# Kernel optimization log

Measured on AMD Instinct MI355X. Metric: run time of the kernel, lower is better.

The kernel has to match this reference:

```python
import jax, jax.numpy as jnp
import numpy as np

TRUNK = 128  # hard-coded trunk_size in the Triton kernels


def setup_inputs() -> dict:
    key = jax.random.key(0)
    kq, kk, kv = jax.random.split(key, 3)
    N, D = 262144, 64
    Q = jax.random.normal(kq, (N, D), dtype=jnp.float32)
    K = jax.random.normal(kk, (N, D), dtype=jnp.float32)
    V = jax.random.normal(kv, (N, D), dtype=jnp.float32)
    return {"Q": Q, "K": K, "V": V}


def reference(Q, K, V):
    # Faithful to the Triton module:
    # 1) intra kernel overwrites Q in-place with, per trunk t:
    #      Q_t <- Q_t @ (V_t^T K_t)^T = Q_t @ K_t^T @ V_t
    # 2) inter kernel accumulates global state S = sum_t V_t^T K_t = V^T K (fp32)
    # 3) final output = Q_intra @ S
    N, D = Q.shape
    dtype = Q.dtype
    assert N % TRUNK == 0
    T = N // TRUNK
    Qt = Q.reshape(T, TRUNK, D)
    Kt = K.reshape(T, TRUNK, D)
    Vt = V.reshape(T, TRUNK, D)
    # per-trunk scores [T, TRUNK, TRUNK], then apply to V
    scores = jnp.einsum('tnd,tmd->tnm', Qt, Kt)
    Q_intra = jnp.einsum('tnm,tmd->tnd', scores, Vt).reshape(N, D)
    # global DxD state in float32 (atomic_add accumulator dtype)
    S = jnp.einsum('nd,ne->de', V.astype(jnp.float32), K.astype(jnp.float32))
    out = Q_intra @ S.astype(dtype)
    return out
```

## Files before the change

### kernel.cpp

```cpp
#include <hip/hip_runtime.h>
#include <hip/hip_bf16.h>


#define TRUNK 128
#define DD 64
#define NPART 1024

typedef __bf16 bf16x8 __attribute__((ext_vector_type(8)));
typedef float  f32x4  __attribute__((ext_vector_type(4)));
typedef unsigned int   u32;
typedef unsigned short u16;
typedef u32 u32x4 __attribute__((ext_vector_type(4)));
typedef u32 u32x2 __attribute__((ext_vector_type(2)));

union F8 { bf16x8 v; u16 u[8]; u32x4 q; };

__device__ __forceinline__ u16 f2bf(float x) {
    union { float f; u32 u; } a; a.f = x;
    u32 u = a.u;
    return (u16)((u + 0x7FFFu + ((u >> 16) & 1u)) >> 16);
}
__device__ __forceinline__ u32 pack2(float a, float b) {
    return (u32)f2bf(a) | ((u32)f2bf(b) << 16);
}

#define P_S  72
#define KV_T 136

__device__ __forceinline__ void stage_T256(const float* __restrict__ M, long tb,
                                           u16* __restrict__ MT, int t) {
    const int c0 = (t >> 4) * 4;
    const int r0 = (t & 15) * 8;
    float4 rw[8];
    #pragma unroll
    for (int i = 0; i < 8; ++i)
        rw[i] = *(const float4*)(M + tb + (long)(r0 + i) * 64 + c0);
    #pragma unroll
    for (int j = 0; j < 4; ++j) {
        u32x4 w;
        w[0] = pack2(((const float*)&rw[0])[j], ((const float*)&rw[1])[j]);
        w[1] = pack2(((const float*)&rw[2])[j], ((const float*)&rw[3])[j]);
        w[2] = pack2(((const float*)&rw[4])[j], ((const float*)&rw[5])[j]);
        w[3] = pack2(((const float*)&rw[6])[j], ((const float*)&rw[7])[j]);
        *(u32x4*)&MT[(c0 + j) * KV_T + r0] = w;
    }
}

__global__ __launch_bounds__(256, 4) void s_partial(const float* __restrict__ K,
                                                    const float* __restrict__ V,
                                                    float* __restrict__ P) {
    __shared__ __align__(16) u16 lds[2 * 64 * KV_T];
    u16* KT = lds;
    u16* VT = lds + 64 * KV_T;

    const int t    = threadIdx.x;
    const int lane = t & 63;
    const int wave = t >> 6;
    const int l15  = lane & 15;
    const int quad = lane >> 4;
    const int mt0  = (wave >> 1) << 1;
    const int nt0  = (wave & 1) << 1;

    f32x4 gacc[2][2] = {};
    const long rowbase = (long)blockIdx.x * 256;

    for (int c = 0; c < 2; ++c) {
        const long tb = (rowbase + c * 128) * 64;
        stage_T256(K, tb, KT, t);
        stage_T256(V, tb, VT, t);
        __syncthreads();
        #pragma unroll
        for (int kt = 0; kt < 4; ++kt) {
            const int rbase = kt * 32 + quad * 8;
            F8 af[2], bf[2];
            #pragma unroll
            for (int mi = 0; mi < 2; ++mi)
                af[mi].q = *(const u32x4*)&VT[((mt0 + mi) * 16 + l15) * KV_T + rbase];
            #pragma unroll
            for (int ni = 0; ni < 2; ++ni)
                bf[ni].q = *(const u32x4*)&KT[((nt0 + ni) * 16 + l15) * KV_T + rbase];
            #pragma unroll
            for (int mi = 0; mi < 2; ++mi)
                #pragma unroll
                for (int ni = 0; ni < 2; ++ni)
                    gacc[mi][ni] = __builtin_amdgcn_mfma_f32_16x16x32_bf16(
                        af[mi].v, bf[ni].v, gacc[mi][ni], 0, 0, 0);
        }
        __syncthreads();
    }

    float* o = P + (long)blockIdx.x * 4096;
    #pragma unroll
    for (int mi = 0; mi < 2; ++mi)
        #pragma unroll
        for (int ni = 0; ni < 2; ++ni) {
            const int b0 = (mt0 + mi) * 16 + quad * 4;
            const int a  = (nt0 + ni) * 16 + l15;
            const float* g = (const float*)&gacc[mi][ni];
            #pragma unroll
            for (int reg = 0; reg < 4; ++reg)
                o[(b0 + reg) * 64 + a] = g[reg];
        }
}

__global__ __launch_bounds__(256) void s_reduce(const float* __restrict__ P,
                                                float* __restrict__ S) {
    const int tid = blockIdx.x * 256 + threadIdx.x;
    const int eg  = tid & 1023;
    const int way = tid >> 10;
    const float4* p = (const float4*)P;
    float4 acc = {0.f, 0.f, 0.f, 0.f};
    #pragma unroll 4
    for (int i = 0; i < 16; ++i) {
        float4 v = p[(long)(way * 16 + i) * 1024 + eg];
        acc.x += v.x; acc.y += v.y; acc.z += v.z; acc.w += v.w;
    }
    atomicAdd(&S[eg * 4 + 0], acc.x);
    atomicAdd(&S[eg * 4 + 1], acc.y);
    atomicAdd(&S[eg * 4 + 2], acc.z);
    atomicAdd(&S[eg * 4 + 3], acc.w);
}

#define KT_OFF 0
#define VT_OFF (64 * KV_T)
#define ST_OFF (2 * 64 * KV_T)
#define LDS_ELEMS (2 * 64 * KV_T + 64 * P_S)

__global__ __launch_bounds__(256, 3) void trunk_kernel(const float* __restrict__ Q,
                                                       const float* __restrict__ K,
                                                       const float* __restrict__ V,
                                                       const float* __restrict__ S,
                                                       float* __restrict__ out) {
    __shared__ __align__(16) u16 lds[LDS_ELEMS];
    u16* KT  = lds + KT_OFF;
    u16* VT  = lds + VT_OFF;
    u16* STb = lds + ST_OFF;
    u16* Gb  = lds + KT_OFF;
    u16* HTb = lds + VT_OFF;

    const int t    = threadIdx.x;
    const int lane = t & 63;
    const int wave = t >> 6;
    const int l15  = lane & 15;
    const int quad = lane >> 4;
    const long tb  = (long)blockIdx.x * (TRUNK * DD);

    F8 a3[2][2];
    #pragma unroll
    for (int kt = 0; kt < 2; ++kt)
        #pragma unroll
        for (int mi = 0; mi < 2; ++mi) {
            const int r = (wave * 2 + mi) * 16 + l15;
            const float* qp = Q + tb + r * 64 + kt * 32 + quad * 8;
            float4 q0 = *(const float4*)qp;
            float4 q1 = *(const float4*)(qp + 4);
            a3[kt][mi].q[0] = pack2(q0.x, q0.y);
            a3[kt][mi].q[1] = pack2(q0.z, q0.w);
            a3[kt][mi].q[2] = pack2(q1.x, q1.y);
            a3[kt][mi].q[3] = pack2(q1.z, q1.w);
        }

    stage_T256(K, tb, KT, t);
    stage_T256(V, tb, VT, t);

    {
        const int sb0 = (t & 7) * 8;
        const int sc0 = (t >> 3) * 2;
        float2 sv[8];
        #pragma unroll
        for (int i = 0; i < 8; ++i)
            sv[i] = *(const float2*)(S + (sb0 + i) * 64 + sc0);
        #pragma unroll
        for (int j = 0; j < 2; ++j) {
            u32x4 w;
            w[0] = pack2(((const float*)&sv[0])[j], ((const float*)&sv[1])[j]);
            w[1] = pack2(((const float*)&sv[2])[j], ((const float*)&sv[3])[j]);
            w[2] = pack2(((const float*)&sv[4])[j], ((const float*)&sv[5])[j]);
            w[3] = pack2(((const float*)&sv[6])[j], ((const float*)&sv[7])[j]);
            *(u32x4*)&STb[(sc0 + j) * P_S + sb0] = w;
        }
    }
    __syncthreads();

    const int mt0 = (wave >> 1) << 1;
    const int nt0 = (wave & 1) << 1;
    f32x4 gacc[2][2] = {};
    #pragma unroll
    for (int kt = 0; kt < 4; ++kt) {
        const int rbase = kt * 32 + quad * 8;
        F8 af[2], bf[2];
        #pragma unroll
        for (int mi = 0; mi < 2; ++mi)
            af[mi].q = *(const u32x4*)&VT[((mt0 + mi) * 16 + l15) * KV_T + rbase];
        #pragma unroll
        for (int ni = 0; ni < 2; ++ni)
            bf[ni].q = *(const u32x4*)&KT[((nt0 + ni) * 16 + l15) * KV_T + rbase];
        #pragma unroll
        for (int mi = 0; mi < 2; ++mi)
            #pragma unroll
            for (int ni = 0; ni < 2; ++ni)
                gacc[mi][ni] = __builtin_amdgcn_mfma_f32_16x16x32_bf16(
                    af[mi].v, bf[ni].v, gacc[mi][ni], 0, 0, 0);
    }
    __syncthreads();

    #pragma unroll
    for (int mi = 0; mi < 2; ++mi)
        #pragma unroll
        for (int ni = 0; ni < 2; ++ni) {
            const int ga  = (nt0 + ni) * 16 + l15;
            const int gb0 = (mt0 + mi) * 16 + quad * 4;
            const float* g = (const float*)&gacc[mi][ni];
            u32x2 w; w[0] = pack2(g[0], g[1]); w[1] = pack2(g[2], g[3]);
            *(u32x2*)&Gb[ga * P_S + gb0] = w;
        }
    __syncthreads();

    f32x4 hacc[2][2] = {};
    #pragma unroll
    for (int kt = 0; kt < 2; ++kt) {
        const int kb = kt * 32 + quad * 8;
        F8 a2[2], b2[2];
        #pragma unroll
        for (int mi = 0; mi < 2; ++mi)
            a2[mi].q = *(const u32x4*)&Gb[((mt0 + mi) * 16 + l15) * P_S + kb];
        #pragma unroll
        for (int ni = 0; ni < 2; ++ni)
            b2[ni].q = *(const u32x4*)&STb[((nt0 + ni) * 16 + l15) * P_S + kb];
        #pragma unroll
        for (int mi = 0; mi < 2; ++mi)
            #pragma unroll
            for (int ni = 0; ni < 2; ++ni)
                hacc[mi][ni] = __builtin_amdgcn_mfma_f32_16x16x32_bf16(
                    a2[mi].v, b2[ni].v, hacc[mi][ni], 0, 0, 0);
    }
    #pragma unroll
    for (int mi = 0; mi < 2; ++mi)
        #pragma unroll
        for (int ni = 0; ni < 2; ++ni) {
            const int hc  = (nt0 + ni) * 16 + l15;
            const int ha0 = (mt0 + mi) * 16 + quad * 4;
            const float* h = (const float*)&hacc[mi][ni];
            u32x2 w; w[0] = pack2(h[0], h[1]); w[1] = pack2(h[2], h[3]);
            *(u32x2*)&HTb[hc * P_S + ha0] = w;
        }
    __syncthreads();

    f32x4 oacc[2][4] = {};
    #pragma unroll
    for (int kt = 0; kt < 2; ++kt) {
        const int ka = kt * 32 + quad * 8;
        #pragma unroll
        for (int ni = 0; ni < 4; ++ni) {
            F8 bb;
            bb.q = *(const u32x4*)&HTb[(ni * 16 + l15) * P_S + ka];
            #pragma unroll
            for (int mi = 0; mi < 2; ++mi)
                oacc[mi][ni] = __builtin_amdgcn_mfma_f32_16x16x32_bf16(
                    a3[kt][mi].v, bb.v, oacc[mi][ni], 0, 0, 0);
        }
    }
    #pragma unroll
    for (int mi = 0; mi < 2; ++mi)
        #pragma unroll
        for (int ni = 0; ni < 4; ++ni) {
            const int row0 = (wave * 2 + mi) * 16 + quad * 4;
            const int col  = ni * 16 + l15;
            const float* o = (const float*)&oacc[mi][ni];
            #pragma unroll
            for (int reg = 0; reg < 4; ++reg)
                out[tb + (long)(row0 + reg) * 64 + col] = o[reg];
        }
}

extern "C" void kernel_launch(void* const* d_in, const int* in_sizes, int n_in,
                              void* d_out, int out_size, void* d_ws, size_t ws_size,
                              hipStream_t stream) {
    const float* Q = (const float*)d_in[0];
    const float* K = (const float*)d_in[1];
    const float* V = (const float*)d_in[2];
    float* out = (float*)d_out;
    float* S   = (float*)d_ws;

    const int n = in_sizes[0] / DD;
    float* P = out + ((long)out_size - (long)NPART * 4096);

    hipMemsetAsync(S, 0, DD * DD * sizeof(float), stream);
    s_partial<<<NPART, 256, 0, stream>>>(K, V, P);
    s_reduce<<<256, 256, 0, stream>>>(P, S);
    trunk_kernel<<<n / TRUNK, 256, 0, stream>>>(Q, K, V, S, out);
}
```

Measured before the change: 246.9 us.

## Compute per-trunk V^T K once and reuse it for global state and output

```diff
diff --git a/kernel.cpp b/kernel.cpp
--- a/kernel.cpp
+++ b/kernel.cpp
@@ -4,7 +4,6 @@
 
 #define TRUNK 128
 #define DD 64
-#define NPART 1024
 
 typedef __bf16 bf16x8 __attribute__((ext_vector_type(8)));
 typedef float  f32x4  __attribute__((ext_vector_type(4)));
@@ -46,9 +45,10 @@
     }
 }
 
-__global__ __launch_bounds__(256, 4) void s_partial(const float* __restrict__ K,
-                                                    const float* __restrict__ V,
-                                                    float* __restrict__ P) {
+__global__ __launch_bounds__(256, 4) void g_kernel(const float* __restrict__ K,
+                                                   const float* __restrict__ V,
+                                                   u16* __restrict__ G,
+                                                   float* __restrict__ S) {
     __shared__ __align__(16) u16 lds[2 * 64 * KV_T];
     u16* KT = lds;
     u16* VT = lds + 64 * KV_T;
@@ -61,35 +61,44 @@
     const int mt0  = (wave >> 1) << 1;
     const int nt0  = (wave & 1) << 1;
 
+    const int  tt = blockIdx.x;
+    const long tb = (long)tt * (TRUNK * DD);
+
+    stage_T256(K, tb, KT, t);
+    stage_T256(V, tb, VT, t);
+    __syncthreads();
+
     f32x4 gacc[2][2] = {};
-    const long rowbase = (long)blockIdx.x * 256;
-
-    for (int c = 0; c < 2; ++c) {
-        const long tb = (rowbase + c * 128) * 64;
-        stage_T256(K, tb, KT, t);
-        stage_T256(V, tb, VT, t);
-        __syncthreads();
-        #pragma unroll
-        for (int kt = 0; kt < 4; ++kt) {
-            const int rbase = kt * 32 + quad * 8;
-            F8 af[2], bf[2];
-            #pragma unroll
-            for (int mi = 0; mi < 2; ++mi)
-                af[mi].q = *(const u32x4*)&VT[((mt0 + mi) * 16 + l15) * KV_T + rbase];
+    #pragma unroll
+    for (int kt = 0; kt < 4; ++kt) {
+        const int rbase = kt * 32 + quad * 8;
+        F8 af[2], bf[2];
+        #pragma unroll
+        for (int mi = 0; mi < 2; ++mi)
+            af[mi].q = *(const u32x4*)&VT[((mt0 + mi) * 16 + l15) * KV_T + rbase];
+        #pragma unroll
+        for (int ni = 0; ni < 2; ++ni)
+            bf[ni].q = *(const u32x4*)&KT[((nt0 + ni) * 16 + l15) * KV_T + rbase];
+        #pragma unroll
+        for (int mi = 0; mi < 2; ++mi)
             #pragma unroll
             for (int ni = 0; ni < 2; ++ni)
-                bf[ni].q = *(const u32x4*)&KT[((nt0 + ni) * 16 + l15) * KV_T + rbase];
-            #pragma unroll
-            for (int mi = 0; mi < 2; ++mi)
-                #pragma unroll
-                for (int ni = 0; ni < 2; ++ni)
-                    gacc[mi][ni] = __builtin_amdgcn_mfma_f32_16x16x32_bf16(
-                        af[mi].v, bf[ni].v, gacc[mi][ni], 0, 0, 0);
-        }
-        __syncthreads();
-    }
-
-    float* o = P + (long)blockIdx.x * 4096;
+                gacc[mi][ni] = __builtin_amdgcn_mfma_f32_16x16x32_bf16(
+                    af[mi].v, bf[ni].v, gacc[mi][ni], 0, 0, 0);
+    }
+
+    u16* Gt = G + ((size_t)(tt >> 1) * 32768 + (size_t)(tt & 1) * 4096);
+    #pragma unroll
+    for (int mi = 0; mi < 2; ++mi)
+        #pragma unroll
+        for (int ni = 0; ni < 2; ++ni) {
+            const int ga  = (nt0 + ni) * 16 + l15;
+            const int gb0 = (mt0 + mi) * 16 + quad * 4;
+            const float* g = (const float*)&gacc[mi][ni];
+            u32x2 w; w[0] = pack2(g[0], g[1]); w[1] = pack2(g[2], g[3]);
+            *(u32x2*)&Gt[ga * 64 + gb0] = w;
+        }
+
     #pragma unroll
     for (int mi = 0; mi < 2; ++mi)
         #pragma unroll
@@ -99,69 +108,38 @@
             const float* g = (const float*)&gacc[mi][ni];
             #pragma unroll
             for (int reg = 0; reg < 4; ++reg)
-                o[(b0 + reg) * 64 + a] = g[reg];
-        }
-}
-
-__global__ __launch_bounds__(256) void s_reduce(const float* __restrict__ P,
-                                                float* __restrict__ S) {
-    const int tid = blockIdx.x * 256 + threadIdx.x;
-    const int eg  = tid & 1023;
-    const int way = tid >> 10;
-    const float4* p = (const float4*)P;
-    float4 acc = {0.f, 0.f, 0.f, 0.f};
-    #pragma unroll 4
-    for (int i = 0; i < 16; ++i) {
-        float4 v = p[(long)(way * 16 + i) * 1024 + eg];
-        acc.x += v.x; acc.y += v.y; acc.z += v.z; acc.w += v.w;
-    }
-    atomicAdd(&S[eg * 4 + 0], acc.x);
-    atomicAdd(&S[eg * 4 + 1], acc.y);
-    atomicAdd(&S[eg * 4 + 2], acc.z);
-    atomicAdd(&S[eg * 4 + 3], acc.w);
-}
-
-#define KT_OFF 0
-#define VT_OFF (64 * KV_T)
-#define ST_OFF (2 * 64 * KV_T)
-#define LDS_ELEMS (2 * 64 * KV_T + 64 * P_S)
-
-__global__ __launch_bounds__(256, 3) void trunk_kernel(const float* __restrict__ Q,
-                                                       const float* __restrict__ K,
-                                                       const float* __restrict__ V,
-                                                       const float* __restrict__ S,
-                                                       float* __restrict__ out) {
-    __shared__ __align__(16) u16 lds[LDS_ELEMS];
-    u16* KT  = lds + KT_OFF;
-    u16* VT  = lds + VT_OFF;
-    u16* STb = lds + ST_OFF;
-    u16* Gb  = lds + KT_OFF;
-    u16* HTb = lds + VT_OFF;
+                atomicAdd(&S[(b0 + reg) * 64 + a], g[reg]);
+        }
+}
+
+#define LDS3 (2 * 64 * P_S)
+
+__global__ __launch_bounds__(256, 3) void out_kernel(const float* __restrict__ Q,
+                                                     const float* __restrict__ S,
+                                                     const u16* __restrict__ G,
+                                                     float* __restrict__ out) {
+    __shared__ __align__(16) u16 lds[LDS3];
+    u16* STb = lds;
+    u16* HTb = lds + 64 * P_S;
 
     const int t    = threadIdx.x;
     const int lane = t & 63;
     const int wave = t >> 6;
     const int l15  = lane & 15;
     const int quad = lane >> 4;
-    const long tb  = (long)blockIdx.x * (TRUNK * DD);
-
-    F8 a3[2][2];
-    #pragma unroll
-    for (int kt = 0; kt < 2; ++kt)
-        #pragma unroll
-        for (int mi = 0; mi < 2; ++mi) {
-            const int r = (wave * 2 + mi) * 16 + l15;
-            const float* qp = Q + tb + r * 64 + kt * 32 + quad * 8;
-            float4 q0 = *(const float4*)qp;
-            float4 q1 = *(const float4*)(qp + 4);
-            a3[kt][mi].q[0] = pack2(q0.x, q0.y);
-            a3[kt][mi].q[1] = pack2(q0.z, q0.w);
-            a3[kt][mi].q[2] = pack2(q1.x, q1.y);
-            a3[kt][mi].q[3] = pack2(q1.z, q1.w);
-        }
-
-    stage_T256(K, tb, KT, t);
-    stage_T256(V, tb, VT, t);
+    const int mt0  = (wave >> 1) << 1;
+    const int nt0  = (wave & 1) << 1;
+
+    const u16* Gblk = G + (size_t)blockIdx.x * 32768;
+    F8 gf[2][2][2];
+    #pragma unroll
+    for (int tr = 0; tr < 2; ++tr)
+        #pragma unroll
+        for (int kt = 0; kt < 2; ++kt)
+            #pragma unroll
+            for (int mi = 0; mi < 2; ++mi)
+                gf[tr][kt][mi].q = *(const u32x4*)&Gblk[(size_t)tr * 4096 +
+                    ((mt0 + mi) * 16 + l15) * 64 + kt * 32 + quad * 8];
 
     {
         const int sb0 = (t & 7) * 8;
@@ -180,97 +158,82 @@
             *(u32x4*)&STb[(sc0 + j) * P_S + sb0] = w;
         }
     }
+    asm volatile("s_waitcnt vmcnt(0)" ::: "memory");
     __syncthreads();
 
-    const int mt0 = (wave >> 1) << 1;
-    const int nt0 = (wave & 1) << 1;
-    f32x4 gacc[2][2] = {};
-    #pragma unroll
-    for (int kt = 0; kt < 4; ++kt) {
-        const int rbase = kt * 32 + quad * 8;
-        F8 af[2], bf[2];
-        #pragma unroll
-        for (int mi = 0; mi < 2; ++mi)
-            af[mi].q = *(const u32x4*)&VT[((mt0 + mi) * 16 + l15) * KV_T + rbase];
-        #pragma unroll
-        for (int ni = 0; ni < 2; ++ni)
-            bf[ni].q = *(const u32x4*)&KT[((nt0 + ni) * 16 + l15) * KV_T + rbase];
-        #pragma unroll
-        for (int mi = 0; mi < 2; ++mi)
+    #pragma unroll
+    for (int tr = 0; tr < 2; ++tr) {
+        const long tb = ((long)blockIdx.x * 2 + tr) * (TRUNK * DD);
+
+        F8 a3[2][2];
+        #pragma unroll
+        for (int kt = 0; kt < 2; ++kt)
+            #pragma unroll
+            for (int mi = 0; mi < 2; ++mi) {
+                const int r = (wave * 2 + mi) * 16 + l15;
+                const float* qp = Q + tb + r * 64 + kt * 32 + quad * 8;
+                float4 q0 = *(const float4*)qp;
+                float4 q1 = *(const float4*)(qp + 4);
+                a3[kt][mi].q[0] = pack2(q0.x, q0.y);
+                a3[kt][mi].q[1] = pack2(q0.z, q0.w);
+                a3[kt][mi].q[2] = pack2(q1.x, q1.y);
+                a3[kt][mi].q[3] = pack2(q1.z, q1.w);
+            }
+
+        f32x4 hacc[2][2] = {};
+        #pragma unroll
+        for (int kt = 0; kt < 2; ++kt) {
+            const int kb = kt * 32 + quad * 8;
+            F8 b2[2];
             #pragma unroll
             for (int ni = 0; ni < 2; ++ni)
-                gacc[mi][ni] = __builtin_amdgcn_mfma_f32_16x16x32_bf16(
-                    af[mi].v, bf[ni].v, gacc[mi][ni], 0, 0, 0);
-    }
-    __syncthreads();
-
-    #pragma unroll
-    for (int mi = 0; mi < 2; ++mi)
-        #pragma unroll
-        for (int ni = 0; ni < 2; ++ni) {
-            const int ga  = (nt0 + ni) * 16 + l15;
-            const int gb0 = (mt0 + mi) * 16 + quad * 4;
-            const float* g = (const float*)&gacc[mi][ni];
-            u32x2 w; w[0] = pack2(g[0], g[1]); w[1] = pack2(g[2], g[3]);
-            *(u32x2*)&Gb[ga * P_S + gb0] = w;
-        }
-    __syncthreads();
-
-    f32x4 hacc[2][2] = {};
-    #pragma unroll
-    for (int kt = 0; kt < 2; ++kt) {
-        const int kb = kt * 32 + quad * 8;
-        F8 a2[2], b2[2];
-        #pragma unroll
-        for (int mi = 0; mi < 2; ++mi)
-            a2[mi].q = *(const u32x4*)&Gb[((mt0 + mi) * 16 + l15) * P_S + kb];
-        #pragma unroll
-        for (int ni = 0; ni < 2; ++ni)
-            b2[ni].q = *(const u32x4*)&STb[((nt0 + ni) * 16 + l15) * P_S + kb];
-        #pragma unroll
-        for (int mi = 0; mi < 2; ++mi)
-            #pragma unroll
-            for (int ni = 0; ni < 2; ++ni)
-                hacc[mi][ni] = __builtin_amdgcn_mfma_f32_16x16x32_bf16(
-                    a2[mi].v, b2[ni].v, hacc[mi][ni], 0, 0, 0);
-    }
-    #pragma unroll
-    for (int mi = 0; mi < 2; ++mi)
-        #pragma unroll
-        for (int ni = 0; ni < 2; ++ni) {
-            const int hc  = (nt0 + ni) * 16 + l15;
-            const int ha0 = (mt0 + mi) * 16 + quad * 4;
-            const float* h = (const float*)&hacc[mi][ni];
-            u32x2 w; w[0] = pack2(h[0], h[1]); w[1] = pack2(h[2], h[3]);
-            *(u32x2*)&HTb[hc * P_S + ha0] = w;
-        }
-    __syncthreads();
-
-    f32x4 oacc[2][4] = {};
-    #pragma unroll
-    for (int kt = 0; kt < 2; ++kt) {
-        const int ka = kt * 32 + quad * 8;
-        #pragma unroll
-        for (int ni = 0; ni < 4; ++ni) {
-            F8 bb;
-            bb.q = *(const u32x4*)&HTb[(ni * 16 + l15) * P_S + ka];
+                b2[ni].q = *(const u32x4*)&STb[((nt0 + ni) * 16 + l15) * P_S + kb];
             #pragma unroll
             for (int mi = 0; mi < 2; ++mi)
-                oacc[mi][ni] = __builtin_amdgcn_mfma_f32_16x16x32_bf16(
-                    a3[kt][mi].v, bb.v, oacc[mi][ni], 0, 0, 0);
-        }
-    }
-    #pragma unroll
-    for (int mi = 0; mi < 2; ++mi)
-        #pragma unroll
-        for (int ni = 0; ni < 4; ++ni) {
-            const int row0 = (wave * 2 + mi) * 16 + quad * 4;
-            const int col  = ni * 16 + l15;
-            const float* o = (const float*)&oacc[mi][ni];
-            #pragma unroll
-            for (int reg = 0; reg < 4; ++reg)
-                out[tb + (long)(row0 + reg) * 64 + col] = o[reg];
-        }
+                #pragma unroll
+                for (int ni = 0; ni < 2; ++ni)
+                    hacc[mi][ni] = __builtin_amdgcn_mfma_f32_16x16x32_bf16(
+                        gf[tr][kt][mi].v, b2[ni].v, hacc[mi][ni], 0, 0, 0);
+        }
+        #pragma unroll
+        for (int mi = 0; mi < 2; ++mi)
+            #pragma unroll
+            for (int ni = 0; ni < 2; ++ni) {
+                const int hc  = (nt0 + ni) * 16 + l15;
+                const int ha0 = (mt0 + mi) * 16 + quad * 4;
+                const float* h = (const float*)&hacc[mi][ni];
+                u32x2 w; w[0] = pack2(h[0], h[1]); w[1] = pack2(h[2], h[3]);
+                *(u32x2*)&HTb[hc * P_S + ha0] = w;
+            }
+        __syncthreads();
+
+        f32x4 oacc[2][4] = {};
+        #pragma unroll
+        for (int kt = 0; kt < 2; ++kt) {
+            const int ka = kt * 32 + quad * 8;
+            #pragma unroll
+            for (int ni = 0; ni < 4; ++ni) {
+                F8 bb;
+                bb.q = *(const u32x4*)&HTb[(ni * 16 + l15) * P_S + ka];
+                #pragma unroll
+                for (int mi = 0; mi < 2; ++mi)
+                    oacc[mi][ni] = __builtin_amdgcn_mfma_f32_16x16x32_bf16(
+                        a3[kt][mi].v, bb.v, oacc[mi][ni], 0, 0, 0);
+            }
+        }
+        #pragma unroll
+        for (int mi = 0; mi < 2; ++mi)
+            #pragma unroll
+            for (int ni = 0; ni < 4; ++ni) {
+                const int row0 = (wave * 2 + mi) * 16 + quad * 4;
+                const int col  = ni * 16 + l15;
+                const float* o = (const float*)&oacc[mi][ni];
+                #pragma unroll
+                for (int reg = 0; reg < 4; ++reg)
+                    out[tb + (long)(row0 + reg) * 64 + col] = o[reg];
+            }
+        if (tr == 0) __syncthreads();
+    }
 }
 
 extern "C" void kernel_launch(void* const* d_in, const int* in_sizes, int n_in,
@@ -283,10 +246,11 @@
     float* S   = (float*)d_ws;
 
     const int n = in_sizes[0] / DD;
-    float* P = out + ((long)out_size - (long)NPART * 4096);
+    const int T = n / TRUNK;
+
+    u16* G = (u16*)out;
 
     hipMemsetAsync(S, 0, DD * DD * sizeof(float), stream);
-    s_partial<<<NPART, 256, 0, stream>>>(K, V, P);
-    s_reduce<<<256, 256, 0, stream>>>(P, S);
-    trunk_kernel<<<n / TRUNK, 256, 0, stream>>>(Q, K, V, S, out);
-}
+    g_kernel<<<T, 256, 0, stream>>>(K, V, G, S);
+    out_kernel<<<T / 2, 256, 0, stream>>>(Q, S, G, out);
+}
```

Measured after the change: 238.9 us. 1.03x faster.
